# Kernel optimization log

Measured on AMD Instinct MI355X. Metric: run time of the kernel, lower is better.

The kernel has to match this reference:

```python
import jax, jax.numpy as jnp
import numpy as np

G, N_PER, H, F_IN, E = 512, 128, 128, 133, 524288
K1, K2, K3 = 103, 83, 67  # ceil(0.8*n) chain: 128->103->83->67 (PyG TopKPooling ratio=0.8)
NEG = 0.01   # leaky_relu default slope
EPS = 1e-5   # BatchNorm eps


def setup_inputs() -> dict:
    key = jax.random.key(0)
    ks = jax.random.split(key, 16)
    e_per = E // G
    # edges are intra-graph: local endpoints + per-graph offset
    src_l = jax.random.randint(ks[0], (G, e_per), 0, N_PER)
    dst_l = jax.random.randint(ks[1], (G, e_per), 0, N_PER)
    off = (jnp.arange(G) * N_PER)[:, None]
    src = (src_l + off).reshape(-1).astype(jnp.int32)
    dst = (dst_l + off).reshape(-1).astype(jnp.int32)
    batch = jnp.repeat(jnp.arange(G, dtype=jnp.int32), N_PER)

    def rn(k, shape, scale=0.05):
        return jax.random.normal(k, shape, dtype=jnp.float32) * scale

    return dict(
        x=jax.random.normal(ks[2], (G * N_PER, F_IN), dtype=jnp.float32),
        src=src, dst=dst, batch=batch,
        W1=rn(ks[3], (F_IN, H)), b1=jnp.zeros((H,), jnp.float32),
        W2=rn(ks[4], (H, H)), b2=jnp.zeros((H,), jnp.float32),
        W3=rn(ks[5], (H, H)), b3=jnp.zeros((H,), jnp.float32),
        p1=rn(ks[6], (H,), 0.1), p2=rn(ks[7], (H,), 0.1), p3=rn(ks[8], (H,), 0.1),
        lin1_W=rn(ks[9], (2 * H, 1024)), lin1_b=jnp.zeros((1024,), jnp.float32),
        lin2_W=rn(ks[10], (1024, 64)), lin2_b=jnp.zeros((64,), jnp.float32),
        lin3_W=rn(ks[11], (64, 2)), lin3_b=jnp.zeros((2,), jnp.float32),
        bn1_g=jnp.ones((1024,), jnp.float32), bn1_b=jnp.zeros((1024,), jnp.float32),
        bn1_rm=jnp.zeros((1024,), jnp.float32), bn1_rv=jnp.ones((1024,), jnp.float32),
        bn2_g=jnp.ones((64,), jnp.float32), bn2_b=jnp.zeros((64,), jnp.float32),
        bn2_rm=jnp.zeros((64,), jnp.float32), bn2_rv=jnp.ones((64,), jnp.float32),
    )


def _gcn(x, W, b, src, dst, em, n_nodes):
    # GCNConv with self-loops & symmetric norm; em masks edges removed by pooling.
    deg = jax.ops.segment_sum(em, dst, num_segments=n_nodes) + 1.0  # +1 self loop
    dis = jax.lax.rsqrt(deg)
    h = x @ W
    coef = dis[src] * dis[dst] * em                      # [E]
    agg = jax.ops.segment_sum(h[src] * coef[:, None], dst, num_segments=n_nodes)
    return agg + h * (1.0 / deg)[:, None] + b            # self-loop term: deg_i^-1 * h_i


def _topk(x, p, src, dst, em, n_per, k):
    # TopKPooling: score = x@p/||p||, keep top-k per graph, gate by tanh(score).
    g = x.shape[0] // n_per
    score = (x @ p) / jnp.linalg.norm(p)                 # [g*n_per]
    vals, idx = jax.lax.top_k(score.reshape(g, n_per), k)  # [g,k]
    xk = jnp.take_along_axis(x.reshape(g, n_per, -1), idx[:, :, None], axis=1)
    x_new = (xk * jnp.tanh(vals)[:, :, None]).reshape(g * k, -1)
    # remap surviving edges; drop (mask) edges touching removed nodes
    remap = jnp.full((g * n_per,), -1, jnp.int32)
    gperm = (jnp.arange(g, dtype=jnp.int32)[:, None] * n_per + idx.astype(jnp.int32)).reshape(-1)
    remap = remap.at[gperm].set(jnp.arange(g * k, dtype=jnp.int32))
    s2, d2 = remap[src], remap[dst]
    ok = (s2 >= 0) & (d2 >= 0)
    return x_new, jnp.where(ok, s2, 0), jnp.where(ok, d2, 0), em * ok.astype(em.dtype)


def _readout(x, g):
    xg = x.reshape(g, -1, x.shape[-1])
    return jnp.concatenate([xg.max(axis=1), xg.mean(axis=1)], axis=-1)  # [g, 2H]


def _lrelu(v):
    return jax.nn.leaky_relu(v, NEG)


def _bn(v, gam, bet, rm, rv):  # eval-mode BatchNorm1d (running stats)
    return (v - rm) * jax.lax.rsqrt(rv + EPS) * gam + bet


def _forward(x, src, dst, W1, b1, W2, b2, W3, b3, p1, p2, p3,
             lin1_W, lin1_b, lin2_W, lin2_b, lin3_W, lin3_b,
             bn1_g, bn1_b, bn1_rm, bn1_rv, bn2_g, bn2_b, bn2_rm, bn2_rv):
    em = jnp.ones(src.shape, jnp.float32)
    h = _lrelu(_gcn(x, W1, b1, src, dst, em, G * N_PER))
    h, src, dst, em = _topk(h, p1, src, dst, em, N_PER, K1)
    r1 = _readout(h, G)
    h = _lrelu(_gcn(h, W2, b2, src, dst, em, G * K1))
    h, src, dst, em = _topk(h, p2, src, dst, em, K1, K2)
    r2 = _readout(h, G)
    h = _lrelu(_gcn(h, W3, b3, src, dst, em, G * K2))
    h, src, dst, em = _topk(h, p3, src, dst, em, K2, K3)
    r3 = _readout(h, G)
    z = r1 + r2 + r3                                      # [G, 2H]
    z = _bn(_lrelu(z @ lin1_W + lin1_b), bn1_g, bn1_b, bn1_rm, bn1_rv)
    z = _bn(_lrelu(z @ lin2_W + lin2_b), bn2_g, bn2_b, bn2_rm, bn2_rv)
    # dropout p=0.5 is identity in eval mode
    return z @ lin3_W + lin3_b                            # [G, num_classes]


def reference(x, src, dst, batch, W1, b1, W2, b2, W3, b3, p1, p2, p3,
              lin1_W, lin1_b, lin2_W, lin2_b, lin3_W, lin3_b,
              bn1_g, bn1_b, bn1_rm, bn1_rv, bn2_g, bn2_b, bn2_rm, bn2_rv):
    # batch is implicit in the regular [G, n_per] layout; kept for signature parity.
    return _forward(x, src, dst, W1, b1, W2, b2, W3, b3, p1, p2, p3,
                    lin1_W, lin1_b, lin2_W, lin2_b, lin3_W, lin3_b,
                    bn1_g, bn1_b, bn1_rm, bn1_rv, bn2_g, bn2_b, bn2_rm, bn2_rv)
```

## Files before the change

kernel.cpp:

```cpp
#include <hip/hip_runtime.h>

#define NEGS 0.01f
#define BNEPS 1e-5f

typedef short bf16x8 __attribute__((ext_vector_type(8)));
typedef float f32x4 __attribute__((ext_vector_type(4)));

__device__ __forceinline__ void split2(float v, short& hi, short& lo) {
    unsigned u = __float_as_uint(v);
    unsigned r = (u + 0x7FFFu + ((u >> 16) & 1u)) >> 16;
    hi = (short)r;
    float hf = __uint_as_float(r << 16);
    float l = v - hf;
    unsigned ul = __float_as_uint(l);
    lo = (short)((ul + 0x7FFFu + ((ul >> 16) & 1u)) >> 16);
}

__global__ __launch_bounds__(256) void split_all(
    const float* __restrict__ W1, const float* __restrict__ W2,
    const float* __restrict__ W3, const float* __restrict__ L1,
    short* __restrict__ h1, short* __restrict__ l1,
    short* __restrict__ h2, short* __restrict__ l2,
    short* __restrict__ h3, short* __restrict__ l3,
    short* __restrict__ h4, short* __restrict__ l4)
{
    int idx = blockIdx.x * 256 + threadIdx.x;
    const float* B; short *H, *L; int K, N, K32, loc;
    if (idx < 20480)      { B = W1; H = h1; L = l1; K = 133; N = 128;  K32 = 160; loc = idx; }
    else if (idx < 36864) { B = W2; H = h2; L = l2; K = 128; N = 128;  K32 = 128; loc = idx - 20480; }
    else if (idx < 53248) { B = W3; H = h3; L = l3; K = 128; N = 128;  K32 = 128; loc = idx - 36864; }
    else                  { B = L1; H = h4; L = l4; K = 256; N = 1024; K32 = 256; loc = idx - 53248; }
    int n = loc % N, k = loc / N;
    float v = (k < K) ? B[(long)k * N + n] : 0.f;
    short hi, lo; split2(v, hi, lo);
    H[(long)n * K32 + k] = hi;
    L[(long)n * K32 + k] = lo;
}

template<int KCH, int VEC, int EPI>
__global__ __launch_bounds__(256) void mfma_gemm(
    const float* __restrict__ A, const short* __restrict__ Bh_t,
    const short* __restrict__ Bl_t, float* __restrict__ C,
    int M, int N, int K,
    const float* __restrict__ bias, const float* __restrict__ bng,
    const float* __restrict__ bnb, const float* __restrict__ bnrm,
    const float* __restrict__ bnrv)
{
    constexpr int K32 = KCH * 32;
    __shared__ short Ahs[64 * 40], Als[64 * 40];
    __shared__ short Bhs[128 * 40], Bls[128 * 40];

    const int tid = threadIdx.x;
    const int bm = blockIdx.y * 64, bn = blockIdx.x * 128;
    const int lane = tid & 63, w = tid >> 6, wm = w >> 1, wn = w & 1;
    const int lm = lane & 15, lk = (lane >> 4) * 8;

    const int arow = tid >> 2, akl = (tid & 3) * 8;
    const int brow = tid & 127, bhl = tid >> 7;
    const short* bsrc = bhl ? Bl_t : Bh_t;
    short* bdst = bhl ? Bls : Bhs;

    const f32x4 zz = {0.f, 0.f, 0.f, 0.f};
    f32x4 acc[2][4];
#pragma unroll
    for (int i = 0; i < 2; ++i)
#pragma unroll
        for (int j = 0; j < 4; ++j) acc[i][j] = zz;

    for (int c = 0; c < KCH; ++c) {
        float av[8];
        if constexpr (VEC == 4) {
            const float4 v0 = *(const float4*)&A[(long)(bm + arow) * K + c * 32 + akl];
            const float4 v1 = *(const float4*)&A[(long)(bm + arow) * K + c * 32 + akl + 4];
            av[0] = v0.x; av[1] = v0.y; av[2] = v0.z; av[3] = v0.w;
            av[4] = v1.x; av[5] = v1.y; av[6] = v1.z; av[7] = v1.w;
        } else {
#pragma unroll
            for (int j = 0; j < 8; ++j) {
                int k = c * 32 + akl + j;
                av[j] = (k < K) ? A[(long)(bm + arow) * K + k] : 0.f;
            }
        }
        bf16x8 h8, l8;
#pragma unroll
        for (int j = 0; j < 8; ++j) { short h_, l_; split2(av[j], h_, l_); h8[j] = h_; l8[j] = l_; }
        *(bf16x8*)&Ahs[arow * 40 + akl] = h8;
        *(bf16x8*)&Als[arow * 40 + akl] = l8;
        const long bbase = (long)(bn + brow) * K32 + c * 32;
#pragma unroll
        for (int j = 0; j < 4; ++j)
            *(bf16x8*)&bdst[brow * 40 + j * 8] = *(const bf16x8*)&bsrc[bbase + j * 8];
        __syncthreads();

        bf16x8 ah0 = *(const bf16x8*)&Ahs[(wm * 32 + lm) * 40 + lk];
        bf16x8 ah1 = *(const bf16x8*)&Ahs[(wm * 32 + 16 + lm) * 40 + lk];
        bf16x8 al0 = *(const bf16x8*)&Als[(wm * 32 + lm) * 40 + lk];
        bf16x8 al1 = *(const bf16x8*)&Als[(wm * 32 + 16 + lm) * 40 + lk];
#pragma unroll
        for (int nt = 0; nt < 4; ++nt) {
            bf16x8 bh = *(const bf16x8*)&Bhs[(wn * 64 + nt * 16 + lm) * 40 + lk];
            bf16x8 bl = *(const bf16x8*)&Bls[(wn * 64 + nt * 16 + lm) * 40 + lk];
            acc[0][nt] = __builtin_amdgcn_mfma_f32_16x16x32_bf16(ah0, bh, acc[0][nt], 0, 0, 0);
            acc[1][nt] = __builtin_amdgcn_mfma_f32_16x16x32_bf16(ah1, bh, acc[1][nt], 0, 0, 0);
            acc[0][nt] = __builtin_amdgcn_mfma_f32_16x16x32_bf16(ah0, bl, acc[0][nt], 0, 0, 0);
            acc[1][nt] = __builtin_amdgcn_mfma_f32_16x16x32_bf16(ah1, bl, acc[1][nt], 0, 0, 0);
            acc[0][nt] = __builtin_amdgcn_mfma_f32_16x16x32_bf16(al0, bh, acc[0][nt], 0, 0, 0);
            acc[1][nt] = __builtin_amdgcn_mfma_f32_16x16x32_bf16(al1, bh, acc[1][nt], 0, 0, 0);
        }
        __syncthreads();
    }

#pragma unroll
    for (int mt = 0; mt < 2; ++mt) {
        int r0 = bm + wm * 32 + mt * 16 + (lane >> 4) * 4;
#pragma unroll
        for (int nt = 0; nt < 4; ++nt) {
            int col = bn + wn * 64 + nt * 16 + lm;
            float bi = 0.f, sc_ = 1.f, rm_ = 0.f, bb_ = 0.f;
            if (EPI == 1) {
                bi = bias[col];
                sc_ = (1.0f / sqrtf(bnrv[col] + BNEPS)) * bng[col];
                rm_ = bnrm[col]; bb_ = bnb[col];
            }
#pragma unroll
            for (int r = 0; r < 4; ++r) {
                float v = acc[mt][nt][r];
                if (EPI == 1) {
                    v += bi;
                    v = v >= 0.f ? v : NEGS * v;
                    v = (v - rm_) * sc_ + bb_;
                }
                C[(long)(r0 + r) * N + col] = v;
            }
        }
    }
}

template<int NC, int KK, bool FIRST, bool LAST, bool ACCUM>
__global__ __launch_bounds__(1024, 8) void gcn_topk(
    float* __restrict__ h,
    const int* __restrict__ srcIn, const int* __restrict__ dstIn,
    int* eS, int* eD, float* eM,
    const float* __restrict__ bias, const float* __restrict__ p,
    float* __restrict__ x_new,
    float* __restrict__ z)
{
    __shared__ float h_s[NC][128];
    __shared__ float2 csr[1024];
    __shared__ int   head[NC];
    __shared__ float deg_s[NC], dis_s[NC], invd_s[NC];
    __shared__ float sc[128];
    __shared__ int   id[128];
    __shared__ float gate[KK];
    __shared__ float b_s[128], p_s[128];
    __shared__ int   remap_l[NC];
    __shared__ float pnorm;

    const int g = blockIdx.x, tid = threadIdx.x, lane = tid & 63;
    const float NINF = -__builtin_inff();

    int es_r, ed_r; float em_r;
    {
        int eg = g * 1024 + tid;
        if (FIRST) { es_r = srcIn[eg] & 127; ed_r = dstIn[eg] & 127; em_r = 1.f; }
        else       { es_r = eS[eg];          ed_r = eD[eg];          em_r = eM[eg]; }
    }

    {
        const float4* hp = (const float4*)(h + (long)g * NC * 128);
        float4* h4 = (float4*)&h_s[0][0];
        for (int i = tid; i < NC * 32; i += 1024) h4[i] = hp[i];
    }
    if (tid < 128) { b_s[tid] = bias[tid]; p_s[tid] = p[tid]; sc[tid] = 0.f; }
    for (int i = tid; i < NC; i += 1024) { deg_s[i] = 1.f; head[i] = 0; }
    __syncthreads();

    if (tid < 64) {
        float s = p_s[tid] * p_s[tid] + p_s[tid + 64] * p_s[tid + 64];
#pragma unroll
        for (int o = 32; o; o >>= 1) s += __shfl_xor(s, o, 64);
        if (tid == 0) pnorm = sqrtf(s);
    }
    const bool live = FIRST || (em_r != 0.f);
    if (live) {
        atomicAdd(&deg_s[ed_r], em_r);
        atomicAdd(&head[ed_r], 1);
    }
    __syncthreads();

    for (int i = tid; i < NC; i += 1024) {
        float d = deg_s[i];
        dis_s[i] = 1.0f / sqrtf(d);
        invd_s[i] = 1.0f / d;
    }
    if (tid < 64) {
        int c0 = head[tid];
        int c1 = (tid + 64 < NC) ? head[tid + 64] : 0;
        int s0 = c0, s1 = c1;
#pragma unroll
        for (int o = 1; o < 64; o <<= 1) { int t = __shfl_up(s0, o, 64); if (lane >= o) s0 += t; }
        int tot0 = __shfl(s0, 63, 64);
#pragma unroll
        for (int o = 1; o < 64; o <<= 1) { int t = __shfl_up(s1, o, 64); if (lane >= o) s1 += t; }
        s1 += tot0;
        head[tid] = s0 - c0;
        if (tid + 64 < NC) head[tid + 64] = s1 - c1;
    }
    __syncthreads();

    if (live) {
        int slot = atomicAdd(&head[ed_r], 1);
        csr[slot] = make_float2(__int_as_float(es_r), dis_s[es_r] * dis_s[ed_r] * em_r);
    }
    __syncthreads();

    {
        const int f = tid & 127, grp = tid >> 7;
        for (int nd = grp; nd < NC; nd += 8) {
            int kb = nd ? head[nd - 1] : 0;
            int ke = head[nd];
            float acc = 0.f;
            for (int k = kb; k < ke; ++k) {
                float2 rec = csr[k];
                acc += h_s[__float_as_int(rec.x)][f] * rec.y;
            }
            float v = acc + h_s[nd][f] * invd_s[nd] + b_s[f];
            v = v >= 0.f ? v : NEGS * v;
            h[((long)g * NC + nd) * 128 + f] = v;
            float ps = v * p_s[f];
#pragma unroll
            for (int o = 32; o; o >>= 1) ps += __shfl_xor(ps, o, 64);
            if (lane == 0) atomicAdd(&sc[nd], ps);
        }
    }
    __syncthreads();

    if (tid < 128) {
        if (tid < NC) { sc[tid] = sc[tid] / pnorm; id[tid] = tid; }
        else          { sc[tid] = NINF; id[tid] = 0x7fffffff; }
    }
    __syncthreads();

    for (int size = 2; size <= 128; size <<= 1) {
        for (int stride = size >> 1; stride > 0; stride >>= 1) {
            if (tid < 64) {
                int i = 2 * stride * (tid / stride) + (tid % stride);
                int j = i + stride;
                float si_ = sc[i], sj_ = sc[j];
                int ii = id[i], ij = id[j];
                bool iFirst = (si_ > sj_) || (si_ == sj_ && ii < ij);
                bool descRegion = ((i & size) == 0);
                bool doSwap = descRegion ? !iFirst : iFirst;
                if (doSwap) { sc[i] = sj_; sc[j] = si_; id[i] = ij; id[j] = ii; }
            }
            __syncthreads();
        }
    }

    for (int j = tid; j < KK; j += 1024) gate[j] = tanhf(sc[j]);
    if constexpr (!LAST) {
        for (int i = tid; i < NC; i += 1024) remap_l[i] = -1;
    }
    __syncthreads();
    if constexpr (!LAST) {
        for (int j = tid; j < KK; j += 1024) remap_l[id[j]] = j;
    }
    __syncthreads();

    if constexpr (!LAST) {
        int s2 = remap_l[es_r], d2 = remap_l[ed_r];
        bool ok = (s2 >= 0) && (d2 >= 0);
        eS[g * 1024 + tid] = ok ? s2 : 0;
        eD[g * 1024 + tid] = ok ? d2 : 0;
        eM[g * 1024 + tid] = ok ? em_r : 0.f;
    }

    float* pmax = (float*)&csr[0];
    float* psum = pmax + 1024;
    {
        const int f = tid & 127, jj = tid >> 7;
        float rmx = NINF, rsm = 0.f;
        for (int j = jj; j < KK; j += 8) {
            float v = h[((long)g * NC + id[j]) * 128 + f] * gate[j];
            if constexpr (!LAST) x_new[((long)g * KK + j) * 128 + f] = v;
            rmx = fmaxf(rmx, v);
            rsm += v;
        }
        pmax[jj * 128 + f] = rmx; psum[jj * 128 + f] = rsm;
    }
    __syncthreads();

    if (tid < 128) {
        float m = pmax[tid], s = psum[tid];
#pragma unroll
        for (int jj = 1; jj < 8; ++jj) { m = fmaxf(m, pmax[jj * 128 + tid]); s += psum[jj * 128 + tid]; }
        float mean = s / (float)KK;
        if constexpr (ACCUM) {
            z[g * 256 + tid] += m;
            z[g * 256 + 128 + tid] += mean;
        } else {
            z[g * 256 + tid] = m;
            z[g * 256 + 128 + tid] = mean;
        }
    }
}

__global__ __launch_bounds__(256) void mlp_tail(
    const float* __restrict__ t1,
    const float* __restrict__ W2, const float* __restrict__ b2v,
    const float* __restrict__ g2, const float* __restrict__ bb2,
    const float* __restrict__ rm2, const float* __restrict__ rv2,
    const float* __restrict__ W3, const float* __restrict__ b3v,
    float* __restrict__ out)
{
    __shared__ float t1s[1024];
    __shared__ float part[4][64];
    __shared__ float t2s[64];
    const int row = blockIdx.x, tid = threadIdx.x;

    for (int i = tid; i < 1024; i += 256) t1s[i] = t1[(long)row * 1024 + i];
    __syncthreads();

    int c = tid & 63, seg = tid >> 6;
    float s = 0.f;
    for (int k = seg * 256; k < seg * 256 + 256; ++k)
        s = fmaf(t1s[k], W2[k * 64 + c], s);
    part[seg][c] = s;
    __syncthreads();

    if (tid < 64) {
        float v = part[0][c] + part[1][c] + part[2][c] + part[3][c] + b2v[c];
        v = v >= 0.f ? v : NEGS * v;
        v = (v - rm2[c]) * (1.0f / sqrtf(rv2[c] + BNEPS)) * g2[c] + bb2[c];
        t2s[c] = v;
    }
    __syncthreads();

    if (tid < 128) {
        int cc = tid >> 6, k = tid & 63;
        float prod = t2s[k] * W3[k * 2 + cc];
#pragma unroll
        for (int o = 32; o; o >>= 1) prod += __shfl_xor(prod, o, 64);
        if (k == 0) out[row * 2 + cc] = prod + b3v[cc];
    }
}

extern "C" void kernel_launch(void* const* d_in, const int* in_sizes, int n_in,
                              void* d_out, int out_size, void* d_ws, size_t ws_size,
                              hipStream_t stream)
{
    const float* x    = (const float*)d_in[0];
    const int*   src  = (const int*)d_in[1];
    const int*   dst  = (const int*)d_in[2];
    const float* W1   = (const float*)d_in[4];
    const float* b1   = (const float*)d_in[5];
    const float* W2   = (const float*)d_in[6];
    const float* b2   = (const float*)d_in[7];
    const float* W3   = (const float*)d_in[8];
    const float* b3   = (const float*)d_in[9];
    const float* p1   = (const float*)d_in[10];
    const float* p2   = (const float*)d_in[11];
    const float* p3   = (const float*)d_in[12];
    const float* l1W  = (const float*)d_in[13];
    const float* l1b  = (const float*)d_in[14];
    const float* l2W  = (const float*)d_in[15];
    const float* l2b  = (const float*)d_in[16];
    const float* l3W  = (const float*)d_in[17];
    const float* l3b  = (const float*)d_in[18];
    const float* bn1g = (const float*)d_in[19];
    const float* bn1b = (const float*)d_in[20];
    const float* bn1rm= (const float*)d_in[21];
    const float* bn1rv= (const float*)d_in[22];
    const float* bn2g = (const float*)d_in[23];
    const float* bn2b = (const float*)d_in[24];
    const float* bn2rm= (const float*)d_in[25];
    const float* bn2rv= (const float*)d_in[26];
    float* out = (float*)d_out;

    float* ws = (float*)d_ws;
    size_t o = 0;
    float* h_pre = ws + o; o += 65536L * 128;
    float* x_cur = ws + o; o += 52736L * 128;
    float* z     = ws + o; o += 512L * 256;
    float* t1    = ws + o; o += 512L * 1024;
    int*   eSA   = (int*)(ws + o); o += 524288;
    int*   eDA   = (int*)(ws + o); o += 524288;
    float* emA   = ws + o; o += 524288;
    short* sp = (short*)(ws + o);
    short* h1s = sp;
    short* l1s = h1s + 20480;
    short* h2s = l1s + 20480;
    short* l2s = h2s + 16384;
    short* h3s = l2s + 16384;
    short* l3s = h3s + 16384;
    short* h4s = l3s + 16384;
    short* l4s = h4s + 262144;

    split_all<<<1232, 256, 0, stream>>>(W1, W2, W3, l1W,
        h1s, l1s, h2s, l2s, h3s, l3s, h4s, l4s);

    mfma_gemm<5,1,0><<<dim3(1,1024), 256, 0, stream>>>(
        x, h1s, l1s, h_pre, 65536, 128, 133, nullptr, nullptr, nullptr, nullptr, nullptr);
    gcn_topk<128,103,true,false,false><<<512, 1024, 0, stream>>>(
        h_pre, src, dst, eSA, eDA, emA, b1, p1, x_cur, z);

    mfma_gemm<4,4,0><<<dim3(1,824), 256, 0, stream>>>(
        x_cur, h2s, l2s, h_pre, 52736, 128, 128, nullptr, nullptr, nullptr, nullptr, nullptr);
    gcn_topk<103,83,false,false,true><<<512, 1024, 0, stream>>>(
        h_pre, nullptr, nullptr, eSA, eDA, emA, b2, p2, x_cur, z);

    mfma_gemm<4,4,0><<<dim3(1,664), 256, 0, stream>>>(
        x_cur, h3s, l3s, h_pre, 42496, 128, 128, nullptr, nullptr, nullptr, nullptr, nullptr);
    gcn_topk<83,67,false,true,true><<<512, 1024, 0, stream>>>(
        h_pre, nullptr, nullptr, eSA, eDA, emA, b3, p3, nullptr, z);

    mfma_gemm<8,4,1><<<dim3(8,8), 256, 0, stream>>>(
        z, h4s, l4s, t1, 512, 1024, 256, l1b, bn1g, bn1b, bn1rm, bn1rv);
    mlp_tail<<<512, 256, 0, stream>>>(
        t1, l2W, l2b, bn2g, bn2b, bn2rm, bn2rv, l3W, l3b, out);
}
```

Before: 306.5 us.

## Keep GCN outputs in shared memory, pack edge arrays, single-wave bitonic sort

The GCN activations are now held in registers and written back into the shared h_s tile instead of being stored to global h and re-read for the top-k gather. Edge src/dst/mask are packed into one int per edge (7+7+1 bits), so one array replaces three in the inter-layer edge traffic. The bitonic sort now runs entirely inside the first wavefront with compiler barriers instead of block-wide syncs. Risks are register pressure from the per-thread value array under 1024-thread launch bounds, and relying on single-wave lockstep for correctness of the sort.

Result: faster. 296.5 us (-3.3%).

```diff
diff --git a/kernel.cpp b/kernel.cpp
--- a/kernel.cpp
+++ b/kernel.cpp
@@ -138,9 +138,9 @@
 
 template<int NC, int KK, bool FIRST, bool LAST, bool ACCUM>
 __global__ __launch_bounds__(1024, 8) void gcn_topk(
-    float* __restrict__ h,
+    const float* __restrict__ h_pre,
     const int* __restrict__ srcIn, const int* __restrict__ dstIn,
-    int* eS, int* eD, float* eM,
+    int* ePK,
     const float* __restrict__ bias, const float* __restrict__ p,
     float* __restrict__ x_new,
     float* __restrict__ z)
@@ -158,16 +158,17 @@
 
     const int g = blockIdx.x, tid = threadIdx.x, lane = tid & 63;
     const float NINF = -__builtin_inff();
-
-    int es_r, ed_r; float em_r;
+    constexpr int NITER = (NC + 7) / 8;
+
+    int es_r, ed_r; bool live;
     {
         int eg = g * 1024 + tid;
-        if (FIRST) { es_r = srcIn[eg] & 127; ed_r = dstIn[eg] & 127; em_r = 1.f; }
-        else       { es_r = eS[eg];          ed_r = eD[eg];          em_r = eM[eg]; }
+        if (FIRST) { es_r = srcIn[eg] & 127; ed_r = dstIn[eg] & 127; live = true; }
+        else       { int pk = ePK[eg]; es_r = pk & 127; ed_r = (pk >> 7) & 127; live = (pk >> 14) != 0; }
     }
 
     {
-        const float4* hp = (const float4*)(h + (long)g * NC * 128);
+        const float4* hp = (const float4*)(h_pre + (long)g * NC * 128);
         float4* h4 = (float4*)&h_s[0][0];
         for (int i = tid; i < NC * 32; i += 1024) h4[i] = hp[i];
     }
@@ -181,9 +182,8 @@
         for (int o = 32; o; o >>= 1) s += __shfl_xor(s, o, 64);
         if (tid == 0) pnorm = sqrtf(s);
     }
-    const bool live = FIRST || (em_r != 0.f);
     if (live) {
-        atomicAdd(&deg_s[ed_r], em_r);
+        atomicAdd(&deg_s[ed_r], 1.0f);
         atomicAdd(&head[ed_r], 1);
     }
     __syncthreads();
@@ -210,27 +210,42 @@
 
     if (live) {
         int slot = atomicAdd(&head[ed_r], 1);
-        csr[slot] = make_float2(__int_as_float(es_r), dis_s[es_r] * dis_s[ed_r] * em_r);
-    }
-    __syncthreads();
-
+        csr[slot] = make_float2(__int_as_float(es_r), dis_s[es_r] * dis_s[ed_r]);
+    }
+    __syncthreads();
+
+    float va[NITER];
     {
         const int f = tid & 127, grp = tid >> 7;
-        for (int nd = grp; nd < NC; nd += 8) {
-            int kb = nd ? head[nd - 1] : 0;
-            int ke = head[nd];
-            float acc = 0.f;
-            for (int k = kb; k < ke; ++k) {
-                float2 rec = csr[k];
-                acc += h_s[__float_as_int(rec.x)][f] * rec.y;
+#pragma unroll
+        for (int i = 0; i < NITER; ++i) {
+            int nd = grp + i * 8;
+            if (nd < NC) {
+                int kb = nd ? head[nd - 1] : 0;
+                int ke = head[nd];
+                float acc = 0.f;
+                for (int k = kb; k < ke; ++k) {
+                    float2 rec = csr[k];
+                    acc += h_s[__float_as_int(rec.x)][f] * rec.y;
+                }
+                float v = acc + h_s[nd][f] * invd_s[nd] + b_s[f];
+                v = v >= 0.f ? v : NEGS * v;
+                va[i] = v;
+                float ps = v * p_s[f];
+#pragma unroll
+                for (int o = 32; o; o >>= 1) ps += __shfl_xor(ps, o, 64);
+                if (lane == 0) atomicAdd(&sc[nd], ps);
             }
-            float v = acc + h_s[nd][f] * invd_s[nd] + b_s[f];
-            v = v >= 0.f ? v : NEGS * v;
-            h[((long)g * NC + nd) * 128 + f] = v;
-            float ps = v * p_s[f];
-#pragma unroll
-            for (int o = 32; o; o >>= 1) ps += __shfl_xor(ps, o, 64);
-            if (lane == 0) atomicAdd(&sc[nd], ps);
+        }
+    }
+    __syncthreads();
+
+    {
+        const int f = tid & 127, grp = tid >> 7;
+#pragma unroll
+        for (int i = 0; i < NITER; ++i) {
+            int nd = grp + i * 8;
+            if (nd < NC) h_s[nd][f] = va[i];
         }
     }
     __syncthreads();
@@ -241,9 +256,9 @@
     }
     __syncthreads();
 
-    for (int size = 2; size <= 128; size <<= 1) {
-        for (int stride = size >> 1; stride > 0; stride >>= 1) {
-            if (tid < 64) {
+    if (tid < 64) {
+        for (int size = 2; size <= 128; size <<= 1) {
+            for (int stride = size >> 1; stride > 0; stride >>= 1) {
                 int i = 2 * stride * (tid / stride) + (tid % stride);
                 int j = i + stride;
                 float si_ = sc[i], sj_ = sc[j];
@@ -252,10 +267,11 @@
                 bool descRegion = ((i & size) == 0);
                 bool doSwap = descRegion ? !iFirst : iFirst;
                 if (doSwap) { sc[i] = sj_; sc[j] = si_; id[i] = ij; id[j] = ii; }
+                __asm__ volatile("" ::: "memory");
             }
-            __syncthreads();
-        }
-    }
+        }
+    }
+    __syncthreads();
 
     for (int j = tid; j < KK; j += 1024) gate[j] = tanhf(sc[j]);
     if constexpr (!LAST) {
@@ -270,9 +286,8 @@
     if constexpr (!LAST) {
         int s2 = remap_l[es_r], d2 = remap_l[ed_r];
         bool ok = (s2 >= 0) && (d2 >= 0);
-        eS[g * 1024 + tid] = ok ? s2 : 0;
-        eD[g * 1024 + tid] = ok ? d2 : 0;
-        eM[g * 1024 + tid] = ok ? em_r : 0.f;
+        int lv = (live && ok) ? 1 : 0;
+        ePK[g * 1024 + tid] = (ok ? s2 : 0) | ((ok ? d2 : 0) << 7) | (lv << 14);
     }
 
     float* pmax = (float*)&csr[0];
@@ -281,7 +296,7 @@
         const int f = tid & 127, jj = tid >> 7;
         float rmx = NINF, rsm = 0.f;
         for (int j = jj; j < KK; j += 8) {
-            float v = h[((long)g * NC + id[j]) * 128 + f] * gate[j];
+            float v = h_s[id[j]][f] * gate[j];
             if constexpr (!LAST) x_new[((long)g * KK + j) * 128 + f] = v;
             rmx = fmaxf(rmx, v);
             rsm += v;
@@ -383,9 +398,7 @@
     float* x_cur = ws + o; o += 52736L * 128;
     float* z     = ws + o; o += 512L * 256;
     float* t1    = ws + o; o += 512L * 1024;
-    int*   eSA   = (int*)(ws + o); o += 524288;
-    int*   eDA   = (int*)(ws + o); o += 524288;
-    float* emA   = ws + o; o += 524288;
+    int*   ePK   = (int*)(ws + o); o += 524288;
     short* sp = (short*)(ws + o);
     short* h1s = sp;
     short* l1s = h1s + 20480;
@@ -402,17 +415,17 @@
     mfma_gemm<5,1,0><<<dim3(1,1024), 256, 0, stream>>>(
         x, h1s, l1s, h_pre, 65536, 128, 133, nullptr, nullptr, nullptr, nullptr, nullptr);
     gcn_topk<128,103,true,false,false><<<512, 1024, 0, stream>>>(
-        h_pre, src, dst, eSA, eDA, emA, b1, p1, x_cur, z);
+        h_pre, src, dst, ePK, b1, p1, x_cur, z);
 
     mfma_gemm<4,4,0><<<dim3(1,824), 256, 0, stream>>>(
         x_cur, h2s, l2s, h_pre, 52736, 128, 128, nullptr, nullptr, nullptr, nullptr, nullptr);
     gcn_topk<103,83,false,false,true><<<512, 1024, 0, stream>>>(
-        h_pre, nullptr, nullptr, eSA, eDA, emA, b2, p2, x_cur, z);
+        h_pre, nullptr, nullptr, ePK, b2, p2, x_cur, z);
 
     mfma_gemm<4,4,0><<<dim3(1,664), 256, 0, stream>>>(
         x_cur, h3s, l3s, h_pre, 42496, 128, 128, nullptr, nullptr, nullptr, nullptr, nullptr);
     gcn_topk<83,67,false,true,true><<<512, 1024, 0, stream>>>(
-        h_pre, nullptr, nullptr, eSA, eDA, emA, b3, p3, nullptr, z);
+        h_pre, nullptr, nullptr, ePK, b3, p3, nullptr, z);
 
     mfma_gemm<8,4,1><<<dim3(8,8), 256, 0, stream>>>(
         z, h4s, l4s, t1, 512, 1024, 256, l1b, bn1g, bn1b, bn1rm, bn1rv);
```
